# Kernel tuning notes

Measured on AMD Instinct MI355X. Metric: run time of the kernel, lower is better.

The kernel has to match this reference:

```python
import jax, jax.numpy as jnp
import numpy as np

B, F, N, D = 4, 5, 2048, 256


def setup_inputs() -> dict:
    key = jax.random.key(0)
    k1, k2 = jax.random.split(key)
    x = jax.random.normal(k1, (B, F, N, D), dtype=jnp.float32)
    y = jax.random.normal(k2, (B, F, N, D), dtype=jnp.float32)
    return {"x": x, "y": y}


def _weight(a, b):
    # pairwise_distance with p=2 in the original is sum((a-b)**2)**(1/(2-1)),
    # i.e. SQUARED euclidean distance (no sqrt). Use gram expansion to avoid
    # materializing the [B,F,N,N,D] difference tensor.
    a2 = jnp.sum(a * a, axis=-1)                      # [B,F,N]
    b2 = jnp.sum(b * b, axis=-1)                      # [B,F,M]
    ab = jnp.einsum('bfnd,bfmd->bfnm', a, b)          # [B,F,N,M]
    d = a2[..., :, None] + b2[..., None, :] - 2.0 * ab  # squared dists
    # min over neighbors (dim=1 of the per-frame matrix), mean over query
    # nodes, then mean over frames -> one scalar per batch element.
    return jnp.mean(jnp.min(d, axis=-1), axis=(-1, -2))  # [B]


def _normalize(f):
    # min/max over the node dim (dim=2), per (batch, frame, feature)
    mn = jnp.min(f, axis=2, keepdims=True)
    mx = jnp.max(f, axis=2, keepdims=True)
    return (f - mn) / (mx - mn)


def reference(x, y):
    wx = 1.0 / (1.0 + _weight(x, y))  # [B]
    wy = 1.0 / (1.0 + _weight(y, x))  # [B]
    nx = _normalize(x)
    ny = _normalize(y)
    return wx[:, None, None, None] * nx + wy[:, None, None, None] * ny
```

## Files before the change

### kernel.cpp

```cpp
#include <hip/hip_runtime.h>

typedef unsigned int u32;
typedef unsigned short u16;
typedef __attribute__((ext_vector_type(8))) short short8;
typedef __attribute__((ext_vector_type(4))) float floatx4;

#define NB 4
#define NF 5
#define NN 2048
#define NDM 256
#define NBF (NB*NF)
#define NBFN (NBF*NN)
#define NBFD (NBF*NDM)

#define AS1 __attribute__((address_space(1)))
#define AS3 __attribute__((address_space(3)))

__device__ u16    g_xb[(size_t)NBF*NN*NDM];
__device__ u16    g_yb[(size_t)NBF*NN*NDM];
__device__ float  g_a2[NBFN];
__device__ float  g_b2[NBFN];
__device__ float  g_rpart[(size_t)4*NBFN];
__device__ float  g_cpart[(size_t)64*NBFN];
__device__ float  g_pmn[2][(size_t)32*NBFD];
__device__ float  g_pmx[2][(size_t)32*NBFD];
__device__ float  g_bfsum[2*NBF];
__device__ float4 g_coef[NBFD];

__device__ __forceinline__ u16 cvt_bf16(float f){
  u32 b = __float_as_uint(f);
  return (u16)((b + 0x7FFFu + ((b >> 16) & 1u)) >> 16);
}
__device__ __forceinline__ float bf2f(short v){
  return __uint_as_float(((u32)(u16)v) << 16);
}
__device__ __forceinline__ void load16(const void* g, void* l){
  __builtin_amdgcn_global_load_lds((AS1 const void*)g, (AS3 void*)l, 16, 0, 0);
}

__global__ void __launch_bounds__(256) k_prep(const float* __restrict__ x,
                                              const float* __restrict__ y){
  __shared__ float sS[64][65];
  __shared__ float sp[4][64];
  __shared__ float4 smn[4][64], smx[4][64];
  int bi = blockIdx.x;
  if (bi == 0 && threadIdx.x < 2*NBF) g_bfsum[threadIdx.x] = 0.f;
  int tensor = bi >= (NBF*32); int rem = bi - tensor*(NBF*32);
  int bf = rem >> 5; int chunk = rem & 31;
  size_t rbase = (size_t)bf*NN + (size_t)chunk*64;
  const float* src = (tensor ? y : x) + rbase*NDM;
  u16*  dst  = (tensor ? g_yb : g_xb) + rbase*NDM;
  float* sums = (tensor ? g_b2 : g_a2) + bf*NN + chunk*64;
  int w = threadIdx.x >> 6, l = threadIdx.x & 63;

  float4 vmn = make_float4(INFINITY,INFINITY,INFINITY,INFINITY);
  float4 vmx = make_float4(-INFINITY,-INFINITY,-INFINITY,-INFINITY);
  for (int i = 0; i < 16; ++i){
    int row = w + 4*i;
    float4 v = ((const float4*)(src + (size_t)row*NDM))[l];
    sS[row][l] = v.x*v.x + v.y*v.y + v.z*v.z + v.w*v.w;
    ((ushort4*)(dst + (size_t)row*NDM))[l] =
        make_ushort4(cvt_bf16(v.x), cvt_bf16(v.y), cvt_bf16(v.z), cvt_bf16(v.w));
    vmn.x = fminf(vmn.x, v.x); vmn.y = fminf(vmn.y, v.y);
    vmn.z = fminf(vmn.z, v.z); vmn.w = fminf(vmn.w, v.w);
    vmx.x = fmaxf(vmx.x, v.x); vmx.y = fmaxf(vmx.y, v.y);
    vmx.z = fmaxf(vmx.z, v.z); vmx.w = fmaxf(vmx.w, v.w);
  }
  smn[w][l] = vmn; smx[w][l] = vmx;
  __syncthreads();
  {
    int row = threadIdx.x & 63, q = threadIdx.x >> 6;
    float p = 0.f;
    #pragma unroll
    for (int i = 0; i < 16; ++i) p += sS[row][q*16 + i];
    sp[q][row] = p;
  }
  __syncthreads();
  if (threadIdx.x < 64)
    sums[threadIdx.x] = sp[0][threadIdx.x] + sp[1][threadIdx.x]
                      + sp[2][threadIdx.x] + sp[3][threadIdx.x];
  if (w == 0){
    float4 a = smn[0][l], b_ = smn[1][l], c = smn[2][l], d = smn[3][l];
    float4 e = smx[0][l], f = smx[1][l], g = smx[2][l], h = smx[3][l];
    float4 mn4 = make_float4(fminf(fminf(a.x,b_.x), fminf(c.x,d.x)),
                             fminf(fminf(a.y,b_.y), fminf(c.y,d.y)),
                             fminf(fminf(a.z,b_.z), fminf(c.z,d.z)),
                             fminf(fminf(a.w,b_.w), fminf(c.w,d.w)));
    float4 mx4 = make_float4(fmaxf(fmaxf(e.x,f.x), fmaxf(g.x,h.x)),
                             fmaxf(fmaxf(e.y,f.y), fmaxf(g.y,h.y)),
                             fmaxf(fmaxf(e.z,f.z), fmaxf(g.z,h.z)),
                             fmaxf(fmaxf(e.w,f.w), fmaxf(g.w,h.w)));
    ((float4*)&g_pmn[tensor][(size_t)chunk*NBFD + bf*NDM])[l] = mn4;
    ((float4*)&g_pmx[tensor][(size_t)chunk*NBFD + bf*NDM])[l] = mx4;
  }
}

__global__ void __launch_bounds__(256, 2) k_gemm(){
  __shared__ u16 Bs[2][128*128];
  __shared__ float b2s[512];
  const int orig = blockIdx.x;
  const int work = (orig & 7)*160 + (orig >> 3);
  const int bf  = work >> 6;
  const int jq  = (work >> 4) & 3;
  const int i0t = work & 15;
  const int i0  = i0t * 128;
  const int t = threadIdx.x;
  const int w = t >> 6, l = t & 63;
  const int quad = l >> 4, c16 = l & 15;
  const int wrow = w * 32;
  const u16* xb = g_xb + (size_t)bf * NN * NDM;
  const u16* yb = g_yb + (size_t)bf * NN * NDM;

  const float* b2 = g_b2 + bf*NN;
  ((float2*)b2s)[t] = ((const float2*)(b2 + jq*512))[t];

  short8 af[2][8];
  #pragma unroll
  for (int mb = 0; mb < 2; ++mb){
    const u16* rp = xb + (size_t)(i0 + wrow + mb*16 + c16) * NDM + quad*8;
    #pragma unroll
    for (int ks = 0; ks < 8; ++ks)
      af[mb][ks] = *(const short8*)(rp + ks*32);
  }
  const float* a2 = g_a2 + bf*NN + i0 + wrow;
  float a2r[2][4];
  #pragma unroll
  for (int mb = 0; mb < 2; ++mb)
    #pragma unroll
    for (int r = 0; r < 4; ++r)
      a2r[mb][r] = a2[mb*16 + quad*4 + r];

  float rm[2][4];
  #pragma unroll
  for (int mb = 0; mb < 2; ++mb)
    #pragma unroll
    for (int r = 0; r < 4; ++r) rm[mb][r] = INFINITY;

  auto stage = [&](int jt, int h, int bb){
    const int j0 = jq*512 + jt*128;
    #pragma unroll
    for (int q = 0; q < 8; ++q){
      const int row = q*16 + w*4 + (l >> 4);
      const int c = (l & 15) ^ (row & 15);
      load16(yb + (size_t)(j0 + row)*NDM + h*128 + c*8,
             &Bs[bb][(q*16 + w*4)*128]);
    }
  };

  int buf = 0;
  stage(0, 0, 0);
  for (int jj = 0; jj < 4; ++jj){
    const int j0 = jq*512 + jj*128;
    floatx4 acc[2][8] = {};
    #pragma unroll
    for (int h = 0; h < 2; ++h){
      __syncthreads();
      const int nit = jj*2 + h + 1;
      if (nit < 8) stage(nit >> 1, nit & 1, buf ^ 1);
      #pragma unroll
      for (int ksl = 0; ksl < 4; ++ksl){
        const int lc = ((ksl*4 + quad) ^ c16) * 8;
        short8 bq[8];
        #pragma unroll
        for (int nb = 0; nb < 8; ++nb)
          bq[nb] = *(const short8*)&Bs[buf][(nb*16 + c16)*128 + lc];
        #pragma unroll
        for (int mb = 0; mb < 2; ++mb)
          #pragma unroll
          for (int nb = 0; nb < 8; ++nb)
            acc[mb][nb] = __builtin_amdgcn_mfma_f32_16x16x32_bf16(af[mb][h*4+ksl], bq[nb], acc[mb][nb], 0, 0, 0);
      }
      buf ^= 1;
    }
    float bcol[8], colm[8];
    #pragma unroll
    for (int nb = 0; nb < 8; ++nb){
      bcol[nb] = b2s[jj*128 + nb*16 + c16];
      colm[nb] = INFINITY;
    }
    #pragma unroll
    for (int mb = 0; mb < 2; ++mb)
      #pragma unroll
      for (int r = 0; r < 4; ++r)
        #pragma unroll
        for (int nb = 0; nb < 8; ++nb){
          float dd = a2r[mb][r] + bcol[nb] - 2.0f * acc[mb][nb][r];
          rm[mb][r] = fminf(rm[mb][r], dd);
          colm[nb] = fminf(colm[nb], dd);
        }
    #pragma unroll
    for (int nb = 0; nb < 8; ++nb){
      float cm = colm[nb];
      cm = fminf(cm, __shfl_xor(cm, 16, 64));
      cm = fminf(cm, __shfl_xor(cm, 32, 64));
      if (quad == 0)
        g_cpart[(size_t)(i0t*4 + w)*NBFN + bf*NN + j0 + nb*16 + c16] = cm;
    }
  }
  #pragma unroll
  for (int mb = 0; mb < 2; ++mb)
    #pragma unroll
    for (int r = 0; r < 4; ++r){
      float v = rm[mb][r];
      v = fminf(v, __shfl_xor(v, 1, 64));
      v = fminf(v, __shfl_xor(v, 2, 64));
      v = fminf(v, __shfl_xor(v, 4, 64));
      v = fminf(v, __shfl_xor(v, 8, 64));
      if (c16 == 0)
        g_rpart[(size_t)jq*NBFN + bf*NN + i0 + wrow + mb*16 + quad*4 + r] = v;
    }
}

__global__ void __launch_bounds__(256) k_weight(){
  int bf = blockIdx.x >> 3;
  int chunk = blockIdx.x & 7;
  int i = chunk*256 + threadIdx.x;
  size_t base = (size_t)bf*NN + i;
  float m = INFINITY, c = INFINITY;
  #pragma unroll
  for (int p = 0; p < 4; ++p)  m = fminf(m, g_rpart[(size_t)p*NBFN + base]);
  #pragma unroll
  for (int p = 0; p < 64; ++p) c = fminf(c, g_cpart[(size_t)p*NBFN + base]);
  float srow = m, scol = c;
  #pragma unroll
  for (int mm = 1; mm < 64; mm <<= 1){
    srow += __shfl_xor(srow, mm, 64);
    scol += __shfl_xor(scol, mm, 64);
  }
  __shared__ float pr[4], pcn[4];
  int w = threadIdx.x >> 6, l = threadIdx.x & 63;
  if (l == 0){ pr[w] = srow; pcn[w] = scol; }
  __syncthreads();
  if (threadIdx.x == 0){
    atomicAdd(&g_bfsum[bf],       pr[0]+pr[1]+pr[2]+pr[3]);
    atomicAdd(&g_bfsum[NBF + bf], pcn[0]+pcn[1]+pcn[2]+pcn[3]);
  }
}

__global__ void k_coef(){
  int idx = blockIdx.x * 256 + threadIdx.x;
  int bf = idx >> 8;
  int b = bf / NF;
  float swx = 0.f, swy = 0.f;
  #pragma unroll
  for (int f = 0; f < NF; ++f){
    swx += g_bfsum[b*NF + f];
    swy += g_bfsum[NBF + b*NF + f];
  }
  float wx = 1.0f / (1.0f + swx * (1.0f/(NF*NN)));
  float wy = 1.0f / (1.0f + swy * (1.0f/(NF*NN)));
  float mnx = INFINITY, mxx = -INFINITY, mny = INFINITY, mxy = -INFINITY;
  #pragma unroll
  for (int c = 0; c < 32; ++c){
    mnx = fminf(mnx, g_pmn[0][(size_t)c*NBFD + idx]);
    mxx = fmaxf(mxx, g_pmx[0][(size_t)c*NBFD + idx]);
    mny = fminf(mny, g_pmn[1][(size_t)c*NBFD + idx]);
    mxy = fmaxf(mxy, g_pmx[1][(size_t)c*NBFD + idx]);
  }
  float sx = wx / (mxx - mnx), sy = wy / (mxy - mny);
  g_coef[idx] = make_float4(sx, -sx * mnx, sy, -sy * mny);
}

__global__ void __launch_bounds__(256) k_out(floatx4* __restrict__ out){
  size_t e0 = ((size_t)blockIdx.x * 256 + threadIdx.x) * 8;
  int bf = (int)(e0 >> 19);
  int d0 = (int)(e0 & 255);
  short8 xv = *(const short8*)&g_xb[e0];
  short8 yv = *(const short8*)&g_yb[e0];
  const float4* cf = &g_coef[bf*256 + d0];
  floatx4 o0, o1;
  #pragma unroll
  for (int j = 0; j < 4; ++j){
    float4 c = cf[j];
    o0[j] = c.x * bf2f(xv[j]) + c.y + c.z * bf2f(yv[j]) + c.w;
  }
  #pragma unroll
  for (int j = 0; j < 4; ++j){
    float4 c = cf[4 + j];
    o1[j] = c.x * bf2f(xv[4 + j]) + c.y + c.z * bf2f(yv[4 + j]) + c.w;
  }
  __builtin_nontemporal_store(o0, &out[e0 >> 2]);
  __builtin_nontemporal_store(o1, &out[(e0 >> 2) + 1]);
}

extern "C" void kernel_launch(void* const* d_in, const int* in_sizes, int n_in,
                              void* d_out, int out_size, void* d_ws, size_t ws_size,
                              hipStream_t stream) {
  const float* x = (const float*)d_in[0];
  const float* y = (const float*)d_in[1];
  (void)d_ws; (void)ws_size; (void)in_sizes; (void)n_in; (void)out_size;

  k_prep  <<<dim3(1280), dim3(256), 0, stream>>>(x, y);
  k_gemm  <<<dim3(1280), dim3(256), 0, stream>>>();
  k_weight<<<dim3(160),  dim3(256), 0, stream>>>();
  k_coef  <<<dim3(20),   dim3(256), 0, stream>>>();
  k_out   <<<dim3(5120), dim3(256), 0, stream>>>((floatx4*)d_out);
}
```

Measured before the change: 215.4 us.

## Load GEMM B tiles directly from global into registers instead of LDS

Removes the LDS double-buffered staging of the y tile (global_load_lds plus __syncthreads) and has each wave load its B fragments directly from global memory into registers with ping-pong prefetch. The b2 norms are also read from global instead of LDS, and launch bounds drop to one block per SM. This aims to remove barrier and LDS overhead, but it multiplies global/L2 traffic by the wave count and raises register pressure.

After: 352.1 us. +63.5%, slower.

```diff
diff --git a/kernel.cpp b/kernel.cpp
--- a/kernel.cpp
+++ b/kernel.cpp
@@ -33,9 +33,6 @@
 }
 __device__ __forceinline__ float bf2f(short v){
   return __uint_as_float(((u32)(u16)v) << 16);
-}
-__device__ __forceinline__ void load16(const void* g, void* l){
-  __builtin_amdgcn_global_load_lds((AS1 const void*)g, (AS3 void*)l, 16, 0, 0);
 }
 
 __global__ void __launch_bounds__(256) k_prep(const float* __restrict__ x,
@@ -95,9 +92,7 @@
   }
 }
 
-__global__ void __launch_bounds__(256, 2) k_gemm(){
-  __shared__ u16 Bs[2][128*128];
-  __shared__ float b2s[512];
+__global__ void __launch_bounds__(256, 1) k_gemm(){
   const int orig = blockIdx.x;
   const int work = (orig & 7)*160 + (orig >> 3);
   const int bf  = work >> 6;
@@ -110,9 +105,7 @@
   const int wrow = w * 32;
   const u16* xb = g_xb + (size_t)bf * NN * NDM;
   const u16* yb = g_yb + (size_t)bf * NN * NDM;
-
-  const float* b2 = g_b2 + bf*NN;
-  ((float2*)b2s)[t] = ((const float2*)(b2 + jq*512))[t];
+  const float* b2 = g_b2 + bf*NN + jq*512;
 
   short8 af[2][8];
   #pragma unroll
@@ -136,46 +129,39 @@
     #pragma unroll
     for (int r = 0; r < 4; ++r) rm[mb][r] = INFINITY;
 
-  auto stage = [&](int jt, int h, int bb){
-    const int j0 = jq*512 + jt*128;
-    #pragma unroll
-    for (int q = 0; q < 8; ++q){
-      const int row = q*16 + w*4 + (l >> 4);
-      const int c = (l & 15) ^ (row & 15);
-      load16(yb + (size_t)(j0 + row)*NDM + h*128 + c*8,
-             &Bs[bb][(q*16 + w*4)*128]);
-    }
-  };
-
-  int buf = 0;
-  stage(0, 0, 0);
   for (int jj = 0; jj < 4; ++jj){
     const int j0 = jq*512 + jj*128;
+    const u16* bp = yb + (size_t)(j0 + c16)*NDM + quad*8;
     floatx4 acc[2][8] = {};
-    #pragma unroll
-    for (int h = 0; h < 2; ++h){
-      __syncthreads();
-      const int nit = jj*2 + h + 1;
-      if (nit < 8) stage(nit >> 1, nit & 1, buf ^ 1);
+    short8 b0[8], b1[8];
+    #pragma unroll
+    for (int nb = 0; nb < 8; ++nb)
+      b0[nb] = *(const short8*)(bp + nb*16*NDM);
+    #pragma unroll
+    for (int ksl = 0; ksl < 8; ++ksl){
+      if (ksl < 7){
+        const u16* np = bp + (ksl+1)*32;
+        if ((ksl & 1) == 0){
+          #pragma unroll
+          for (int nb = 0; nb < 8; ++nb)
+            b1[nb] = *(const short8*)(np + nb*16*NDM);
+        } else {
+          #pragma unroll
+          for (int nb = 0; nb < 8; ++nb)
+            b0[nb] = *(const short8*)(np + nb*16*NDM);
+        }
+      }
       #pragma unroll
-      for (int ksl = 0; ksl < 4; ++ksl){
-        const int lc = ((ksl*4 + quad) ^ c16) * 8;
-        short8 bq[8];
+      for (int mb = 0; mb < 2; ++mb)
         #pragma unroll
         for (int nb = 0; nb < 8; ++nb)
-          bq[nb] = *(const short8*)&Bs[buf][(nb*16 + c16)*128 + lc];
-        #pragma unroll
-        for (int mb = 0; mb < 2; ++mb)
-          #pragma unroll
-          for (int nb = 0; nb < 8; ++nb)
-            acc[mb][nb] = __builtin_amdgcn_mfma_f32_16x16x32_bf16(af[mb][h*4+ksl], bq[nb], acc[mb][nb], 0, 0, 0);
-      }
-      buf ^= 1;
+          acc[mb][nb] = __builtin_amdgcn_mfma_f32_16x16x32_bf16(
+              af[mb][ksl], (ksl & 1) ? b1[nb] : b0[nb], acc[mb][nb], 0, 0, 0);
     }
     float bcol[8], colm[8];
     #pragma unroll
     for (int nb = 0; nb < 8; ++nb){
-      bcol[nb] = b2s[jj*128 + nb*16 + c16];
+      bcol[nb] = b2[jj*128 + nb*16 + c16];
       colm[nb] = INFINITY;
     }
     #pragma unroll
```

## Replace partial-min buffers with atomic order-preserving key reductions and fuse finalize kernels

Applied to the files above, without the earlier changes.

The per-chunk row/column min partials and per-chunk min/max partials are replaced by atomicMax on monotonic uint keys that map floats to sortable integers, so results are reduced in place. The separate weight and coef kernels become one 4-block finalize kernel, which decodes the keys, computes the weights and coefficients, and resets the accumulators to zero for the next call. This cuts partial-buffer traffic and one launch, but adds atomic contention in the GEMM epilogue. The finalize step now runs on only 4 blocks, which serializes the sum over 10240 elements per batch. It also relies on the buffers starting at zero on the first call, which __device__ globals are.

Result: slower. 233.8 us (+8.6%).

```diff
diff --git a/kernel.cpp b/kernel.cpp
--- a/kernel.cpp
+++ b/kernel.cpp
@@ -20,11 +20,10 @@
 __device__ u16    g_yb[(size_t)NBF*NN*NDM];
 __device__ float  g_a2[NBFN];
 __device__ float  g_b2[NBFN];
-__device__ float  g_rpart[(size_t)4*NBFN];
-__device__ float  g_cpart[(size_t)64*NBFN];
-__device__ float  g_pmn[2][(size_t)32*NBFD];
-__device__ float  g_pmx[2][(size_t)32*NBFD];
-__device__ float  g_bfsum[2*NBF];
+__device__ u32    g_rk[NBFN];
+__device__ u32    g_ck[NBFN];
+__device__ u32    g_mnk[2][NBFD];
+__device__ u32    g_mxk[2][NBFD];
 __device__ float4 g_coef[NBFD];
 
 __device__ __forceinline__ u16 cvt_bf16(float f){
@@ -36,6 +35,13 @@
 }
 __device__ __forceinline__ void load16(const void* g, void* l){
   __builtin_amdgcn_global_load_lds((AS1 const void*)g, (AS3 void*)l, 16, 0, 0);
+}
+__device__ __forceinline__ u32 fkey(float f){
+  u32 b = __float_as_uint(f);
+  return (b & 0x80000000u) ? ~b : (b | 0x80000000u);
+}
+__device__ __forceinline__ float fdec(u32 k){
+  return __uint_as_float((k & 0x80000000u) ? (k ^ 0x80000000u) : ~k);
 }
 
 __global__ void __launch_bounds__(256) k_prep(const float* __restrict__ x,
@@ -44,7 +50,6 @@
   __shared__ float sp[4][64];
   __shared__ float4 smn[4][64], smx[4][64];
   int bi = blockIdx.x;
-  if (bi == 0 && threadIdx.x < 2*NBF) g_bfsum[threadIdx.x] = 0.f;
   int tensor = bi >= (NBF*32); int rem = bi - tensor*(NBF*32);
   int bf = rem >> 5; int chunk = rem & 31;
   size_t rbase = (size_t)bf*NN + (size_t)chunk*64;
@@ -90,8 +95,15 @@
                              fmaxf(fmaxf(e.y,f.y), fmaxf(g.y,h.y)),
                              fmaxf(fmaxf(e.z,f.z), fmaxf(g.z,h.z)),
                              fmaxf(fmaxf(e.w,f.w), fmaxf(g.w,h.w)));
-    ((float4*)&g_pmn[tensor][(size_t)chunk*NBFD + bf*NDM])[l] = mn4;
-    ((float4*)&g_pmx[tensor][(size_t)chunk*NBFD + bf*NDM])[l] = mx4;
+    u32 base = (u32)bf*NDM + 4*l;
+    atomicMax(&g_mnk[tensor][base+0], ~fkey(mn4.x));
+    atomicMax(&g_mnk[tensor][base+1], ~fkey(mn4.y));
+    atomicMax(&g_mnk[tensor][base+2], ~fkey(mn4.z));
+    atomicMax(&g_mnk[tensor][base+3], ~fkey(mn4.w));
+    atomicMax(&g_mxk[tensor][base+0],  fkey(mx4.x));
+    atomicMax(&g_mxk[tensor][base+1],  fkey(mx4.y));
+    atomicMax(&g_mxk[tensor][base+2],  fkey(mx4.z));
+    atomicMax(&g_mxk[tensor][base+3],  fkey(mx4.w));
   }
 }
 
@@ -194,7 +206,7 @@
       cm = fminf(cm, __shfl_xor(cm, 16, 64));
       cm = fminf(cm, __shfl_xor(cm, 32, 64));
       if (quad == 0)
-        g_cpart[(size_t)(i0t*4 + w)*NBFN + bf*NN + j0 + nb*16 + c16] = cm;
+        atomicMax(&g_ck[bf*NN + j0 + nb*16 + c16], ~fkey(cm));
     }
   }
   #pragma unroll
@@ -207,58 +219,48 @@
       v = fminf(v, __shfl_xor(v, 4, 64));
       v = fminf(v, __shfl_xor(v, 8, 64));
       if (c16 == 0)
-        g_rpart[(size_t)jq*NBFN + bf*NN + i0 + wrow + mb*16 + quad*4 + r] = v;
-    }
-}
-
-__global__ void __launch_bounds__(256) k_weight(){
-  int bf = blockIdx.x >> 3;
-  int chunk = blockIdx.x & 7;
-  int i = chunk*256 + threadIdx.x;
-  size_t base = (size_t)bf*NN + i;
-  float m = INFINITY, c = INFINITY;
-  #pragma unroll
-  for (int p = 0; p < 4; ++p)  m = fminf(m, g_rpart[(size_t)p*NBFN + base]);
-  #pragma unroll
-  for (int p = 0; p < 64; ++p) c = fminf(c, g_cpart[(size_t)p*NBFN + base]);
-  float srow = m, scol = c;
-  #pragma unroll
-  for (int mm = 1; mm < 64; mm <<= 1){
-    srow += __shfl_xor(srow, mm, 64);
-    scol += __shfl_xor(scol, mm, 64);
-  }
-  __shared__ float pr[4], pcn[4];
-  int w = threadIdx.x >> 6, l = threadIdx.x & 63;
-  if (l == 0){ pr[w] = srow; pcn[w] = scol; }
+        atomicMax(&g_rk[bf*NN + i0 + wrow + mb*16 + quad*4 + r], ~fkey(v));
+    }
+}
+
+__global__ void __launch_bounds__(256) k_fin(){
+  const int b = blockIdx.x;
+  const int t = threadIdx.x;
+  __shared__ float sw[2][4];
+  float swx = 0.f, swy = 0.f;
+  #pragma unroll
+  for (int f = 0; f < NF; ++f){
+    const int bf = b*NF + f;
+    #pragma unroll
+    for (int i = 0; i < NN/256; ++i){
+      int idx = bf*NN + i*256 + t;
+      swx += fdec(~g_rk[idx]);
+      swy += fdec(~g_ck[idx]);
+      g_rk[idx] = 0u; g_ck[idx] = 0u;
+    }
+  }
+  #pragma unroll
+  for (int m = 1; m < 64; m <<= 1){
+    swx += __shfl_xor(swx, m, 64);
+    swy += __shfl_xor(swy, m, 64);
+  }
+  int w = t >> 6, l = t & 63;
+  if (l == 0){ sw[0][w] = swx; sw[1][w] = swy; }
   __syncthreads();
-  if (threadIdx.x == 0){
-    atomicAdd(&g_bfsum[bf],       pr[0]+pr[1]+pr[2]+pr[3]);
-    atomicAdd(&g_bfsum[NBF + bf], pcn[0]+pcn[1]+pcn[2]+pcn[3]);
-  }
-}
-
-__global__ void k_coef(){
-  int idx = blockIdx.x * 256 + threadIdx.x;
-  int bf = idx >> 8;
-  int b = bf / NF;
-  float swx = 0.f, swy = 0.f;
+  float SX = sw[0][0] + sw[0][1] + sw[0][2] + sw[0][3];
+  float SY = sw[1][0] + sw[1][1] + sw[1][2] + sw[1][3];
+  float wx = 1.0f / (1.0f + SX * (1.0f/(NF*NN)));
+  float wy = 1.0f / (1.0f + SY * (1.0f/(NF*NN)));
   #pragma unroll
   for (int f = 0; f < NF; ++f){
-    swx += g_bfsum[b*NF + f];
-    swy += g_bfsum[NBF + b*NF + f];
-  }
-  float wx = 1.0f / (1.0f + swx * (1.0f/(NF*NN)));
-  float wy = 1.0f / (1.0f + swy * (1.0f/(NF*NN)));
-  float mnx = INFINITY, mxx = -INFINITY, mny = INFINITY, mxy = -INFINITY;
-  #pragma unroll
-  for (int c = 0; c < 32; ++c){
-    mnx = fminf(mnx, g_pmn[0][(size_t)c*NBFD + idx]);
-    mxx = fmaxf(mxx, g_pmx[0][(size_t)c*NBFD + idx]);
-    mny = fminf(mny, g_pmn[1][(size_t)c*NBFD + idx]);
-    mxy = fmaxf(mxy, g_pmx[1][(size_t)c*NBFD + idx]);
-  }
-  float sx = wx / (mxx - mnx), sy = wy / (mxy - mny);
-  g_coef[idx] = make_float4(sx, -sx * mnx, sy, -sy * mny);
+    const int idx = (b*NF + f)*NDM + t;
+    float mnx = fdec(~g_mnk[0][idx]), mxx = fdec(g_mxk[0][idx]);
+    float mny = fdec(~g_mnk[1][idx]), mxy = fdec(g_mxk[1][idx]);
+    float sx = wx / (mxx - mnx), sy = wy / (mxy - mny);
+    g_coef[idx] = make_float4(sx, -sx * mnx, sy, -sy * mny);
+    g_mnk[0][idx] = 0u; g_mxk[0][idx] = 0u;
+    g_mnk[1][idx] = 0u; g_mxk[1][idx] = 0u;
+  }
 }
 
 __global__ void __launch_bounds__(256) k_out(floatx4* __restrict__ out){
@@ -290,9 +292,8 @@
   const float* y = (const float*)d_in[1];
   (void)d_ws; (void)ws_size; (void)in_sizes; (void)n_in; (void)out_size;
 
-  k_prep  <<<dim3(1280), dim3(256), 0, stream>>>(x, y);
-  k_gemm  <<<dim3(1280), dim3(256), 0, stream>>>();
-  k_weight<<<dim3(160),  dim3(256), 0, stream>>>();
-  k_coef  <<<dim3(20),   dim3(256), 0, stream>>>();
-  k_out   <<<dim3(5120), dim3(256), 0, stream>>>((floatx4*)d_out);
-}
+  k_prep<<<dim3(1280), dim3(256), 0, stream>>>(x, y);
+  k_gemm<<<dim3(1280), dim3(256), 0, stream>>>();
+  k_fin <<<dim3(4),    dim3(256), 0, stream>>>();
+  k_out <<<dim3(5120), dim3(256), 0, stream>>>((floatx4*)d_out);
+}
```
